# Kernel tuning notes

Hardware: AMD Instinct MI355X
Metric: run time of the kernel (lower is better)

Reference implementation:

```python
import jax, jax.numpy as jnp
import numpy as np

H = 8   # heads
C = 64  # per-head channels (gnn_hidden_dim)
HID = H * C  # 512
IN_CH = 6
EMB = 64
U, M = 16, 512
N_NODES = U * M  # 8192
N_EDGES = 131072


def _tconv(x, src, dst, Wq, bq, Wk, bk, Wv, bv, Ws, bs):
    """PyG TransformerConv (concat=True, root_weight=True, beta=False, eval mode)."""
    N = x.shape[0]
    q = (x @ Wq + bq).reshape(N, H, C)
    k = (x @ Wk + bk).reshape(N, H, C)
    v = (x @ Wv + bv).reshape(N, H, C)
    # per-edge attention scores: query at dst (target i), key at src (source j)
    score = jnp.einsum('ehc,ehc->eh', q[dst], k[src]) / jnp.sqrt(jnp.float32(C))
    # segment softmax over incoming edges of each dst node
    mx = jax.ops.segment_max(score, dst, num_segments=N)
    ex = jnp.exp(score - mx[dst])
    denom = jax.ops.segment_sum(ex, dst, num_segments=N)
    alpha = ex / (denom[dst] + 1e-16)  # [E, H]
    msg = alpha[..., None] * v[src]    # [E, H, C]
    out = jax.ops.segment_sum(msg, dst, num_segments=N).reshape(N, HID)
    return out + x @ Ws + bs  # root/skip connection


def setup_inputs() -> dict:
    key = jax.random.key(0)
    ks = iter(jax.random.split(key, 64))
    s = 0.05

    def lin(k, i, o):
        k1, k2 = jax.random.split(k)
        return (jax.random.normal(k1, (i, o), jnp.float32) * s,
                jax.random.normal(k2, (o,), jnp.float32) * s)

    inp = {}
    inp['mission_coords'] = jax.random.uniform(next(ks), (M, 2), jnp.float32)
    inp['uavs_info'] = jax.random.uniform(next(ks), (U, 2), jnp.float32)
    inp['speeds'] = jax.random.uniform(next(ks), (U,), jnp.float32)
    inp['dist_matrix'] = jax.random.uniform(next(ks), (U, M), jnp.float32)
    inp['timetogo_matrix'] = jax.random.uniform(next(ks), (U, M), jnp.float32)
    inp['action_mask'] = jax.random.randint(next(ks), (U, M), 0, 2, jnp.int32)
    inp['edge_index'] = jax.random.randint(next(ks), (2, N_EDGES), 0, N_NODES, jnp.int64)
    inp['batch'] = jnp.zeros((U,), jnp.int64)

    # layer 0 (in=6)
    inp['Wq0'], inp['bq0'] = lin(next(ks), IN_CH, HID)
    inp['Wk0'], inp['bk0'] = lin(next(ks), IN_CH, HID)
    inp['Wv0'], inp['bv0'] = lin(next(ks), IN_CH, HID)
    inp['Ws0'], inp['bs0'] = lin(next(ks), IN_CH, HID)
    # layers 1..3 stacked (in=512)
    for nm in ['Wq', 'Wk', 'Wv', 'Ws']:
        Ws_, bs_ = [], []
        for _ in range(3):
            w, b = lin(next(ks), HID, HID)
            Ws_.append(w); bs_.append(b)
        inp[nm] = jnp.stack(Ws_)
        inp['b' + nm[1:].lower()] = jnp.stack(bs_)
    inp['Wout'], inp['bout'] = lin(next(ks), HID, EMB)
    inp['Wa1'], inp['ba1'] = lin(next(ks), EMB + 3, 128)
    inp['Wa2'], inp['ba2'] = lin(next(ks), 128, 1)
    inp['Wc1'], inp['bc1'] = lin(next(ks), EMB + 3, 128)
    inp['Wc2'], inp['bc2'] = lin(next(ks), 128, 1)
    return inp


def reference(mission_coords, uavs_info, speeds, dist_matrix, timetogo_matrix,
              action_mask, edge_index, batch,
              Wq0, bq0, Wk0, bk0, Wv0, bv0, Ws0, bs0,
              Wq, bq, Wk, bk, Wv, bv, Ws, bs,
              Wout, bout, Wa1, ba1, Wa2, ba2, Wc1, bc1, Wc2, bc2):
    u, m = uavs_info.shape[0], mission_coords.shape[0]
    mc = jnp.broadcast_to(mission_coords[None], (u, m, 2))
    mask_e = action_mask[..., None].astype(jnp.float32)
    sp_e = jnp.broadcast_to(speeds[:, None, None], (u, m, 1))
    x = jnp.concatenate([mc, mask_e, sp_e, dist_matrix[..., None],
                         timetogo_matrix[..., None]], axis=-1).reshape(u * m, IN_CH)
    src, dst = edge_index[0], edge_index[1]
    x = jax.nn.relu(_tconv(x, src, dst, Wq0, bq0, Wk0, bk0, Wv0, bv0, Ws0, bs0))
    for l in range(3):
        x = jax.nn.relu(_tconv(x, src, dst, Wq[l], bq[l], Wk[l], bk[l],
                               Wv[l], bv[l], Ws[l], bs[l]))
    x = x @ Wout + bout  # [U*M, EMB]
    uav_emb = x.reshape(u, m, EMB).sum(axis=1)  # sum pooling over missions
    combined = jnp.concatenate([uavs_info, uav_emb, speeds[:, None]], axis=-1)
    logits = jax.nn.relu(combined @ Wa1 + ba1) @ Wa2 + ba2  # [U, 1]
    action_probs = jax.nn.softmax(logits, axis=-1)
    state_values = (jax.nn.relu(combined @ Wc1 + bc1) @ Wc2 + bc2).squeeze()
    return action_probs, state_values
```

## Files before the change

### kernel.cpp

```cpp
#include <hip/hip_runtime.h>
#include <hip/hip_bf16.h>
#include <math.h>

#define NNODES 8192
#define NEDGES 131072
#define HID    512
#define UU     16
#define MM     512
#define NQKVS  2048

#if __has_builtin(__builtin_amdgcn_cvt_pk_f32_fp8) && __has_builtin(__builtin_amdgcn_cvt_pk_fp8_f32)
#define HAVE_FP8 1
#else
#define HAVE_FP8 0
#endif

#define KSCALE 16.0f
#define KISCALE (0.125f / 16.0f)

typedef __attribute__((ext_vector_type(8))) short bf16x8;
typedef __attribute__((ext_vector_type(4))) float f32x4;
typedef __attribute__((ext_vector_type(2))) float f32x2;

__device__ __forceinline__ float bf2f(ushort u) {
    return __uint_as_float(((unsigned)u) << 16);
}
__device__ __forceinline__ ushort f2bf(float f) {
    unsigned x = __float_as_uint(f);
    return (ushort)((x + 0x7fffu + ((x >> 16) & 1u)) >> 16);
}

__global__ __launch_bounds__(256) void k_wt(
    const float* __restrict__ Wq, const float* __restrict__ Wk,
    const float* __restrict__ Wv, const float* __restrict__ Ws,
    ushort* __restrict__ Wt)
{
    __shared__ float tile[64][65];
    int z = blockIdx.z;
    int l = z >> 2, which = z & 3;
    const float* src = (which == 0 ? Wq : which == 1 ? Wk : which == 2 ? Wv : Ws)
                       + (size_t)l * HID * HID;
    int k0 = blockIdx.x * 64, c0 = blockIdx.y * 64;
    int t = threadIdx.x;
#pragma unroll
    for (int i = 0; i < 16; ++i) {
        int idx = i * 256 + t;
        int r = idx >> 6, c = idx & 63;
        tile[r][c] = src[(size_t)(k0 + r) * HID + c0 + c];
    }
    __syncthreads();
    ushort* dst = Wt + ((size_t)l * NQKVS + which * HID + c0) * HID + k0;
#pragma unroll
    for (int i = 0; i < 16; ++i) {
        int idx = i * 256 + t;
        int r = idx >> 6, c = idx & 63;
        dst[(size_t)r * HID + c] = f2bf(tile[c][r]);
    }
}

__global__ __launch_bounds__(256) void k_bias(
    const float* __restrict__ bq, const float* __restrict__ bk,
    const float* __restrict__ bv, const float* __restrict__ bs,
    float* __restrict__ bcat)
{
    int i = blockIdx.x * 256 + threadIdx.x;
    int l = i >> 11, j = i & 2047;
    int which = j >> 9, jj = j & 511;
    const float* b = which == 0 ? bq : which == 1 ? bk : which == 2 ? bv : bs;
    bcat[i] = b[l * HID + jj];
}

__global__ __launch_bounds__(256) void k_lin0(
    const float* __restrict__ mc, const float* __restrict__ speeds,
    const float* __restrict__ dist, const float* __restrict__ ttg,
    const int* __restrict__ mask,
    const float* __restrict__ Wq0, const float* __restrict__ bq0,
    const float* __restrict__ Wk0, const float* __restrict__ bk0,
    const float* __restrict__ Wv0, const float* __restrict__ bv0,
    const float* __restrict__ Ws0, const float* __restrict__ bs0,
    ushort* __restrict__ Y, unsigned char* __restrict__ Kf8)
{
    int n = blockIdx.x;
    int u = n >> 9, m = n & 511;
    float x[6];
    x[0] = mc[m * 2 + 0];
    x[1] = mc[m * 2 + 1];
    x[2] = (float)mask[u * MM + m];
    x[3] = speeds[u];
    x[4] = dist[u * MM + m];
    x[5] = ttg[u * MM + m];

    int j = threadIdx.x;
    int col0 = j * 8;
    int which = col0 >> 9, jj = col0 & 511;
    const float* W = which == 0 ? Wq0 : which == 1 ? Wk0 : which == 2 ? Wv0 : Ws0;
    const float* b = which == 0 ? bq0 : which == 1 ? bk0 : which == 2 ? bv0 : bs0;
    float s[8];
#pragma unroll
    for (int uu = 0; uu < 8; ++uu) s[uu] = b[jj + uu];
#pragma unroll
    for (int t = 0; t < 6; ++t)
#pragma unroll
        for (int uu = 0; uu < 8; ++uu)
            s[uu] = fmaf(x[t], W[t * HID + jj + uu], s[uu]);
    bf16x8 o8;
#pragma unroll
    for (int uu = 0; uu < 8; ++uu) o8[uu] = (short)f2bf(s[uu]);
    *(bf16x8*)(Y + (size_t)n * NQKVS + col0) = o8;
#if HAVE_FP8
    if (which == 1) {
        int w0 = __builtin_amdgcn_cvt_pk_fp8_f32(s[0] * KSCALE, s[1] * KSCALE, 0, false);
        w0     = __builtin_amdgcn_cvt_pk_fp8_f32(s[2] * KSCALE, s[3] * KSCALE, w0, true);
        int w1 = __builtin_amdgcn_cvt_pk_fp8_f32(s[4] * KSCALE, s[5] * KSCALE, 0, false);
        w1     = __builtin_amdgcn_cvt_pk_fp8_f32(s[6] * KSCALE, s[7] * KSCALE, w1, true);
        uint2 uu2; uu2.x = (unsigned)w0; uu2.y = (unsigned)w1;
        *(uint2*)(Kf8 + (size_t)n * HID + jj) = uu2;
    }
#endif
}

#define GBM 256
#define GBN 256
#define GBK 64
#define MATB 32768
#define BUFB (2 * MATB)

#define VMCNT(n) asm volatile("s_waitcnt vmcnt(" #n ")" ::: "memory")

__device__ __forceinline__ void stage_tile256(
    const ushort* __restrict__ Ag, const ushort* __restrict__ Bg,
    char* __restrict__ buf, int t)
{
#pragma unroll
    for (int h = 0; h < 8; ++h) {
        int slot = h * 512 + t;
        const ushort* src = (h < 4) ? Ag : Bg;
        int s = slot & 2047;
        int row = s >> 3, kqs = s & 7;
        int kq = kqs ^ (row & 7);
        __builtin_amdgcn_global_load_lds(
            (const __attribute__((address_space(1))) void*)(src + (size_t)row * HID + kq * 8),
            (__attribute__((address_space(3))) void*)(buf + slot * 16), 16, 0, 0);
    }
}

__global__ __launch_bounds__(512, 1) void k_gemm(
    const ushort* __restrict__ A,
    const ushort* __restrict__ Bt,
    const float* __restrict__ bias,
    ushort* __restrict__ Y,
    unsigned char* __restrict__ Kf8)
{
    extern __shared__ char lds[];
    const int t = threadIdx.x;
    const int bid = blockIdx.x;
    const int xcd = bid & 7;
    const int ii  = bid >> 3;
    const int mi  = (xcd << 2) | (ii & 3);
    const int ni  = ii >> 2;
    const int m0 = mi * GBM, n0 = ni * GBN;

    const int wid = t >> 6, lane = t & 63;
    const int wr = wid >> 2, wc = wid & 3;
    const int l15 = lane & 15, lkq = lane >> 4;

    f32x4 acc[8][4] = {};

    const ushort* Ab = A + (size_t)m0 * HID;
    const ushort* Bb = Bt + (size_t)n0 * HID;

    stage_tile256(Ab, Bb, lds, t);
    stage_tile256(Ab + GBK, Bb + GBK, lds + BUFB, t);

    const int NKT = HID / GBK;
#pragma unroll
    for (int T = 0; T < NKT; ++T) {
        if (T < NKT - 1) { VMCNT(8); } else { VMCNT(0); }
        __builtin_amdgcn_s_barrier();
        __builtin_amdgcn_sched_barrier(0);
        const char* la = lds + (T & 1) * BUFB;
        const char* lb = la + MATB;
#pragma unroll
        for (int kh = 0; kh < 2; ++kh) {
            const int kq = kh * 4 + lkq;
            const int sw = (kq ^ (l15 & 7)) << 4;
            bf16x8 a[8], b[4];
#pragma unroll
            for (int i = 0; i < 8; ++i)
                a[i] = *(const bf16x8*)(la + (wr * 128 + i * 16 + l15) * 128 + sw);
#pragma unroll
            for (int j = 0; j < 4; ++j)
                b[j] = *(const bf16x8*)(lb + (wc * 64 + j * 16 + l15) * 128 + sw);
            __builtin_amdgcn_s_setprio(1);
#pragma unroll
            for (int i = 0; i < 8; ++i)
#pragma unroll
                for (int j = 0; j < 4; ++j)
                    acc[i][j] = __builtin_amdgcn_mfma_f32_16x16x32_bf16(a[i], b[j], acc[i][j], 0, 0, 0);
            __builtin_amdgcn_s_setprio(0);
        }
        __builtin_amdgcn_s_barrier();
        __builtin_amdgcn_sched_barrier(0);
        if (T + 2 < NKT)
            stage_tile256(Ab + (T + 2) * GBK, Bb + (T + 2) * GBK,
                          lds + (T & 1) * BUFB, t);
    }

    const bool kquad = ((n0 >> 9) == 1);
#pragma unroll
    for (int i = 0; i < 8; ++i) {
        int row = m0 + wr * 128 + i * 16 + lkq * 4;
#pragma unroll
        for (int j = 0; j < 4; ++j) {
            int col = n0 + wc * 64 + j * 16 + l15;
            float bc = bias[col];
            f32x4 r = acc[i][j];
#pragma unroll
            for (int g = 0; g < 4; ++g) {
                float val = r[g] + bc;
                Y[(size_t)(row + g) * NQKVS + col] = f2bf(val);
#if HAVE_FP8
                if (kquad) {
                    int pk = __builtin_amdgcn_cvt_pk_fp8_f32(val * KSCALE, val * KSCALE, 0, false);
                    Kf8[(size_t)(row + g) * HID + (col - 512)] = (unsigned char)(pk & 0xff);
                }
#endif
            }
        }
    }
}

__global__ __launch_bounds__(256) void k_hist(const int* __restrict__ dst, int* __restrict__ cnt)
{
    int e = blockIdx.x * blockDim.x + threadIdx.x;
    if (e < NEDGES) atomicAdd(&cnt[dst[e]], 1);
}

__global__ __launch_bounds__(256) void k_scan(const int* __restrict__ cnt, int* __restrict__ indptr)
{
    __shared__ int sums[256];
    __shared__ int offs[256];
    int t = threadIdx.x;
    int base = t * 32;
    int s = 0;
    for (int i = 0; i < 32; ++i) s += cnt[base + i];
    sums[t] = s;
    __syncthreads();
    if (t == 0) {
        int run = 0;
        for (int i = 0; i < 256; ++i) { offs[i] = run; run += sums[i]; }
    }
    __syncthreads();
    int off = offs[t];
    for (int i = 0; i < 32; ++i) { indptr[base + i] = off; off += cnt[base + i]; }
    if (t == 255) indptr[NNODES] = off;
}

__global__ __launch_bounds__(256) void k_scatter(
    const int* __restrict__ src, const int* __restrict__ dst,
    const int* __restrict__ indptr, int* __restrict__ cursor, int* __restrict__ ssrc)
{
    int e = blockIdx.x * blockDim.x + threadIdx.x;
    if (e >= NEDGES) return;
    int d = dst[e];
    int p = atomicAdd(&cursor[d], 1);
    ssrc[indptr[d] + p] = src[e];
}

__global__ __launch_bounds__(256) void k_attn(
    const int* __restrict__ indptr, const int* __restrict__ ssrc,
    const ushort* __restrict__ Y,
    const unsigned char* __restrict__ Kf8,
    ushort* __restrict__ X)
{
    int n = blockIdx.x * 4 + (threadIdx.x >> 6);
    if (n >= NNODES) return;
    int l = threadIdx.x & 63;
    int cbase = l * 8;
    const ushort* yq = Y + (size_t)n * NQKVS + cbase;
    float qf[8];
    {
        bf16x8 q8 = *(const bf16x8*)yq;
#pragma unroll
        for (int j = 0; j < 8; ++j) qf[j] = bf2f((ushort)q8[j]);
    }
    float mrun = -INFINITY, ssum = 0.f;
    float acc[8] = {};
    int e0 = indptr[n], e1 = indptr[n + 1];
#if HAVE_FP8
    uint2 ka = {}, kb = {};
#else
    bf16x8 ka = {}, kb = {};
#endif
    bf16x8 va = {}, vb = {};
    if (e0 < e1) {
        int s = ssrc[e0];
#if HAVE_FP8
        ka = *(const uint2*)(Kf8 + (size_t)s * HID + cbase);
#else
        ka = *(const bf16x8*)(Y + (size_t)s * NQKVS + 512 + cbase);
#endif
        va = *(const bf16x8*)(Y + (size_t)s * NQKVS + 1024 + cbase);
    }
    if (e0 + 1 < e1) {
        int s = ssrc[e0 + 1];
#if HAVE_FP8
        kb = *(const uint2*)(Kf8 + (size_t)s * HID + cbase);
#else
        kb = *(const bf16x8*)(Y + (size_t)s * NQKVS + 512 + cbase);
#endif
        vb = *(const bf16x8*)(Y + (size_t)s * NQKVS + 1024 + cbase);
    }
    for (int e = e0; e < e1; ++e) {
        auto k8 = ka; bf16x8 v8 = va;
        ka = kb; va = vb;
        int en = e + 2;
        if (en < e1) {
            int s = ssrc[en];
#if HAVE_FP8
            kb = *(const uint2*)(Kf8 + (size_t)s * HID + cbase);
#else
            kb = *(const bf16x8*)(Y + (size_t)s * NQKVS + 512 + cbase);
#endif
            vb = *(const bf16x8*)(Y + (size_t)s * NQKVS + 1024 + cbase);
        }
        float part = 0.f;
#if HAVE_FP8
        {
            f32x2 k01 = __builtin_amdgcn_cvt_pk_f32_fp8((int)k8.x, false);
            f32x2 k23 = __builtin_amdgcn_cvt_pk_f32_fp8((int)k8.x, true);
            f32x2 k45 = __builtin_amdgcn_cvt_pk_f32_fp8((int)k8.y, false);
            f32x2 k67 = __builtin_amdgcn_cvt_pk_f32_fp8((int)k8.y, true);
            part = fmaf(qf[0], k01.x, part); part = fmaf(qf[1], k01.y, part);
            part = fmaf(qf[2], k23.x, part); part = fmaf(qf[3], k23.y, part);
            part = fmaf(qf[4], k45.x, part); part = fmaf(qf[5], k45.y, part);
            part = fmaf(qf[6], k67.x, part); part = fmaf(qf[7], k67.y, part);
        }
#else
#pragma unroll
        for (int j = 0; j < 8; ++j) part = fmaf(qf[j], bf2f((ushort)k8[j]), part);
#endif
        part += __shfl_xor(part, 1);
        part += __shfl_xor(part, 2);
        part += __shfl_xor(part, 4);
#if HAVE_FP8
        float score = part * KISCALE;
#else
        float score = part * 0.125f;
#endif
        float mnew = fmaxf(mrun, score);
        float sc = __expf(mrun - mnew);
        float p = __expf(score - mnew);
        ssum = ssum * sc + p;
#pragma unroll
        for (int j = 0; j < 8; ++j)
            acc[j] = fmaf(acc[j], sc, p * bf2f((ushort)v8[j]));
        mrun = mnew;
    }
    float inv = ssum > 0.f ? 1.f / ssum : 0.f;
    bf16x8 o8;
#pragma unroll
    for (int j = 0; j < 8; ++j) {
        float o = fmaxf(fmaf(acc[j], inv, bf2f(yq[1536 + j])), 0.f);
        o8[j] = (short)f2bf(o);
    }
    *(bf16x8*)(X + (size_t)n * HID + cbase) = o8;
}

__global__ __launch_bounds__(512) void k_pool(const ushort* __restrict__ X, float* __restrict__ xsumP)
{
    int u = blockIdx.x;
    int pp = blockIdx.y;
    int c = threadIdx.x;
    const ushort* base = X + ((size_t)u * MM + pp * 64) * HID + c;
    float s = 0.f;
    for (int m = 0; m < 64; ++m) s += bf2f(base[(size_t)m * HID]);
    xsumP[((size_t)u * 8 + pp) * HID + c] = s;
}

__global__ __launch_bounds__(512) void k_emb(
    const float* __restrict__ xsumP, const float* __restrict__ Wout,
    const float* __restrict__ bout, float* __restrict__ emb)
{
    __shared__ float xs[HID];
    int u = blockIdx.x, c = threadIdx.x;
    float s = 0.f;
#pragma unroll
    for (int p = 0; p < 8; ++p) s += xsumP[((size_t)u * 8 + p) * HID + c];
    xs[c] = s;
    __syncthreads();
    if (c < 64) {
        float a = 0.f;
        for (int i = 0; i < HID; ++i) a = fmaf(xs[i], Wout[i * 64 + c], a);
        emb[u * 64 + c] = a + 512.0f * bout[c];
    }
}

__global__ __launch_bounds__(128) void k_head(
    const float* __restrict__ uavs, const float* __restrict__ speeds,
    const float* __restrict__ emb,
    const float* __restrict__ Wc1, const float* __restrict__ bc1,
    const float* __restrict__ Wc2, const float* __restrict__ bc2,
    float* __restrict__ out)
{
    __shared__ float comb[67];
    __shared__ float red[128];
    int u = blockIdx.x, t = threadIdx.x;
    if (t < 2) comb[t] = uavs[u * 2 + t];
    else if (t < 66) comb[t] = emb[u * 64 + (t - 2)];
    else if (t == 66) comb[t] = speeds[u];
    __syncthreads();
    float a = bc1[t];
    for (int i = 0; i < 67; ++i) a = fmaf(comb[i], Wc1[i * 128 + t], a);
    a = fmaxf(a, 0.f);
    red[t] = a * Wc2[t];
    __syncthreads();
    for (int sft = 64; sft > 0; sft >>= 1) {
        if (t < sft) red[t] += red[t + sft];
        __syncthreads();
    }
    if (t == 0) {
        out[u]      = 1.0f;
        out[16 + u] = red[0] + bc2[0];
    }
}

extern "C" void kernel_launch(void* const* d_in, const int* in_sizes, int n_in,
                              void* d_out, int out_size, void* d_ws, size_t ws_size,
                              hipStream_t stream)
{
    const float* mission_coords = (const float*)d_in[0];
    const float* uavs_info      = (const float*)d_in[1];
    const float* speeds         = (const float*)d_in[2];
    const float* dist_matrix    = (const float*)d_in[3];
    const float* timetogo       = (const float*)d_in[4];
    const int*   action_mask    = (const int*)d_in[5];
    const int*   edge_index     = (const int*)d_in[6];
    const float* Wq0 = (const float*)d_in[8];  const float* bq0 = (const float*)d_in[9];
    const float* Wk0 = (const float*)d_in[10]; const float* bk0 = (const float*)d_in[11];
    const float* Wv0 = (const float*)d_in[12]; const float* bv0 = (const float*)d_in[13];
    const float* Ws0 = (const float*)d_in[14]; const float* bs0 = (const float*)d_in[15];
    const float* Wq  = (const float*)d_in[16]; const float* bq  = (const float*)d_in[17];
    const float* Wk  = (const float*)d_in[18]; const float* bk  = (const float*)d_in[19];
    const float* Wv  = (const float*)d_in[20]; const float* bv  = (const float*)d_in[21];
    const float* Ws  = (const float*)d_in[22]; const float* bs  = (const float*)d_in[23];
    const float* Wout = (const float*)d_in[24]; const float* bout = (const float*)d_in[25];
    const float* Wc1 = (const float*)d_in[30]; const float* bc1 = (const float*)d_in[31];
    const float* Wc2 = (const float*)d_in[32]; const float* bc2 = (const float*)d_in[33];
    float* out = (float*)d_out;

    const int* e_src = edge_index;
    const int* e_dst = edge_index + NEDGES;

    char* p = (char*)d_ws;
    ushort* Ybf = (ushort*)p;  p += (size_t)NNODES * NQKVS * 2;
    ushort* Xbf = (ushort*)p;  p += (size_t)NNODES * HID * 2;
    ushort* Wt  = (ushort*)p;  p += (size_t)3 * NQKVS * HID * 2;
    unsigned char* Kf8 = (unsigned char*)p; p += (size_t)NNODES * HID;
    float* bcat = (float*)p;   p += (size_t)3 * NQKVS * 4;
    float* xsumP = (float*)p;  p += (size_t)UU * 8 * HID * 4;
    float* emb  = (float*)p;   p += (size_t)UU * 64 * 4;
    int* cnt    = (int*)p;     p += (size_t)NNODES * 4;
    int* indptr = (int*)p;     p += (size_t)(NNODES + 1) * 4;
    int* cursor = (int*)p;     p += (size_t)NNODES * 4;
    int* ssrc   = (int*)p;     p += (size_t)NEDGES * 4;

    hipMemsetAsync(cnt, 0, NNODES * sizeof(int), stream);
    hipMemsetAsync(cursor, 0, NNODES * sizeof(int), stream);

    static bool attr_done = false;
    if (!attr_done) {
        hipFuncSetAttribute((const void*)k_gemm,
                            hipFuncAttributeMaxDynamicSharedMemorySize, 131072);
        attr_done = true;
    }

    k_wt<<<dim3(8, 8, 12), 256, 0, stream>>>(Wq, Wk, Wv, Ws, Wt);
    k_bias<<<3 * NQKVS / 256, 256, 0, stream>>>(bq, bk, bv, bs, bcat);
    k_hist<<<NEDGES / 256, 256, 0, stream>>>(e_dst, cnt);
    k_scan<<<1, 256, 0, stream>>>(cnt, indptr);
    k_scatter<<<NEDGES / 256, 256, 0, stream>>>(e_src, e_dst, indptr, cursor, ssrc);

    k_lin0<<<NNODES, 256, 0, stream>>>(mission_coords, speeds, dist_matrix, timetogo,
                                       action_mask, Wq0, bq0, Wk0, bk0, Wv0, bv0,
                                       Ws0, bs0, Ybf, Kf8);
    k_attn<<<NNODES / 4, 256, 0, stream>>>(indptr, ssrc, Ybf, Kf8, Xbf);

    const int ngblocks = (NNODES / GBM) * (NQKVS / GBN);
    for (int l = 0; l < 3; ++l) {
        k_gemm<<<ngblocks, 512, 131072, stream>>>(Xbf, Wt + (size_t)l * NQKVS * HID,
                                                  bcat + l * NQKVS, Ybf, Kf8);
        k_attn<<<NNODES / 4, 256, 0, stream>>>(indptr, ssrc, Ybf, Kf8, Xbf);
    }

    k_pool<<<dim3(UU, 8), 512, 0, stream>>>(Xbf, xsumP);
    k_emb<<<UU, 512, 0, stream>>>(xsumP, Wout, bout, emb);
    k_head<<<UU, 128, 0, stream>>>(uavs_info, speeds, emb, Wc1, bc1, Wc2, bc2, out);
}
```

Before: 281.2 us.

## Shrink GEMM tiles, deepen attention prefetch, fuse small setup and head kernels

The GEMM moves from 256x256x64 tiles with 512 threads and 128KB dynamic LDS to 128x128x32 tiles with 256 threads, static LDS and four blocks per CU, using a new LDS swizzle that interleaves A and B rows. The aim is more blocks in flight and better latency hiding. The cost is less operand reuse per block and more global traffic. The attention loop now prefetches four edges ahead instead of two. Several small launches are also merged: weight transpose with bias concat, embedding with head, and the two memsets into one. The scan is rewritten with wave shuffles.

```diff
diff --git a/kernel.cpp b/kernel.cpp
--- a/kernel.cpp
+++ b/kernel.cpp
@@ -30,18 +30,31 @@
     return (ushort)((x + 0x7fffu + ((x >> 16) & 1u)) >> 16);
 }
 
-__global__ __launch_bounds__(256) void k_wt(
+__global__ __launch_bounds__(256) void k_wtb(
     const float* __restrict__ Wq, const float* __restrict__ Wk,
     const float* __restrict__ Wv, const float* __restrict__ Ws,
-    ushort* __restrict__ Wt)
+    const float* __restrict__ bq, const float* __restrict__ bk,
+    const float* __restrict__ bv, const float* __restrict__ bs,
+    ushort* __restrict__ Wt, float* __restrict__ bcat)
 {
     __shared__ float tile[64][65];
     int z = blockIdx.z;
+    int t = threadIdx.x;
+    if (z == 12) {
+        int id = blockIdx.y * 8 + blockIdx.x;
+        if (id < 24) {
+            int i = id * 256 + t;
+            int l = i >> 11, j = i & 2047;
+            int which = j >> 9, jj = j & 511;
+            const float* b = which == 0 ? bq : which == 1 ? bk : which == 2 ? bv : bs;
+            bcat[i] = b[l * HID + jj];
+        }
+        return;
+    }
     int l = z >> 2, which = z & 3;
     const float* src = (which == 0 ? Wq : which == 1 ? Wk : which == 2 ? Wv : Ws)
                        + (size_t)l * HID * HID;
     int k0 = blockIdx.x * 64, c0 = blockIdx.y * 64;
-    int t = threadIdx.x;
 #pragma unroll
     for (int i = 0; i < 16; ++i) {
         int idx = i * 256 + t;
@@ -56,18 +69,6 @@
         int r = idx >> 6, c = idx & 63;
         dst[(size_t)r * HID + c] = f2bf(tile[c][r]);
     }
-}
-
-__global__ __launch_bounds__(256) void k_bias(
-    const float* __restrict__ bq, const float* __restrict__ bk,
-    const float* __restrict__ bv, const float* __restrict__ bs,
-    float* __restrict__ bcat)
-{
-    int i = blockIdx.x * 256 + threadIdx.x;
-    int l = i >> 11, j = i & 2047;
-    int which = j >> 9, jj = j & 511;
-    const float* b = which == 0 ? bq : which == 1 ? bk : which == 2 ? bv : bs;
-    bcat[i] = b[l * HID + jj];
 }
 
 __global__ __launch_bounds__(256) void k_lin0(
@@ -119,97 +120,99 @@
 #endif
 }
 
-#define GBM 256
-#define GBN 256
-#define GBK 64
-#define MATB 32768
-#define BUFB (2 * MATB)
+#define GBM 128
+#define GBN 128
+#define GBK 32
+#define BUF32 16384
 
 #define VMCNT(n) asm volatile("s_waitcnt vmcnt(" #n ")" ::: "memory")
 
-__device__ __forceinline__ void stage_tile256(
+__device__ __forceinline__ void stage32(
     const ushort* __restrict__ Ag, const ushort* __restrict__ Bg,
     char* __restrict__ buf, int t)
 {
 #pragma unroll
-    for (int h = 0; h < 8; ++h) {
-        int slot = h * 512 + t;
-        const ushort* src = (h < 4) ? Ag : Bg;
-        int s = slot & 2047;
-        int row = s >> 3, kqs = s & 7;
-        int kq = kqs ^ (row & 7);
+    for (int i = 0; i < 4; ++i) {
+        int slot = i * 256 + t;
+        int row  = slot >> 3;
+        int sl8  = slot & 7;
+        int h    = sl8 >> 2;
+        int kqs  = sl8 & 3;
+        int hA   = (row >> 2) & 1;
+        int kq   = kqs ^ (row & 3);
+        const ushort* src = (h == hA ? Ag : Bg) + (size_t)row * HID + kq * 8;
         __builtin_amdgcn_global_load_lds(
-            (const __attribute__((address_space(1))) void*)(src + (size_t)row * HID + kq * 8),
+            (const __attribute__((address_space(1))) void*)src,
             (__attribute__((address_space(3))) void*)(buf + slot * 16), 16, 0, 0);
     }
 }
 
-__global__ __launch_bounds__(512, 1) void k_gemm(
+__global__ __launch_bounds__(256, 4) void k_gemm(
     const ushort* __restrict__ A,
     const ushort* __restrict__ Bt,
     const float* __restrict__ bias,
     ushort* __restrict__ Y,
     unsigned char* __restrict__ Kf8)
 {
-    extern __shared__ char lds[];
+    __shared__ char lds[2 * BUF32];
     const int t = threadIdx.x;
     const int bid = blockIdx.x;
     const int xcd = bid & 7;
     const int ii  = bid >> 3;
-    const int mi  = (xcd << 2) | (ii & 3);
-    const int ni  = ii >> 2;
+    const int mi  = (xcd << 3) | (ii & 7);
+    const int ni  = ii >> 3;
     const int m0 = mi * GBM, n0 = ni * GBN;
 
     const int wid = t >> 6, lane = t & 63;
-    const int wr = wid >> 2, wc = wid & 3;
+    const int wr = wid >> 1, wc = wid & 1;
     const int l15 = lane & 15, lkq = lane >> 4;
 
-    f32x4 acc[8][4] = {};
+    f32x4 acc[4][4] = {};
 
     const ushort* Ab = A + (size_t)m0 * HID;
     const ushort* Bb = Bt + (size_t)n0 * HID;
 
-    stage_tile256(Ab, Bb, lds, t);
-    stage_tile256(Ab + GBK, Bb + GBK, lds + BUFB, t);
+    stage32(Ab, Bb, lds, t);
+    stage32(Ab + GBK, Bb + GBK, lds + BUF32, t);
 
     const int NKT = HID / GBK;
 #pragma unroll
     for (int T = 0; T < NKT; ++T) {
-        if (T < NKT - 1) { VMCNT(8); } else { VMCNT(0); }
+        if (T < NKT - 1) { VMCNT(4); } else { VMCNT(0); }
         __builtin_amdgcn_s_barrier();
         __builtin_amdgcn_sched_barrier(0);
-        const char* la = lds + (T & 1) * BUFB;
-        const char* lb = la + MATB;
-#pragma unroll
-        for (int kh = 0; kh < 2; ++kh) {
-            const int kq = kh * 4 + lkq;
-            const int sw = (kq ^ (l15 & 7)) << 4;
-            bf16x8 a[8], b[4];
-#pragma unroll
-            for (int i = 0; i < 8; ++i)
-                a[i] = *(const bf16x8*)(la + (wr * 128 + i * 16 + l15) * 128 + sw);
+        const char* lb_ = lds + (T & 1) * BUF32;
+        bf16x8 a[4], b[4];
+#pragma unroll
+        for (int i = 0; i < 4; ++i) {
+            int row = wr * 64 + i * 16 + l15;
+            a[i] = *(const bf16x8*)(lb_ + row * 128 + ((row & 4) << 4)
+                                    + ((lkq ^ (row & 3)) << 4));
+        }
+#pragma unroll
+        for (int j = 0; j < 4; ++j) {
+            int row = wc * 64 + j * 16 + l15;
+            b[j] = *(const bf16x8*)(lb_ + row * 128 + (((row & 4) ^ 4) << 4)
+                                    + ((lkq ^ (row & 3)) << 4));
+        }
+        __builtin_amdgcn_s_setprio(1);
+#pragma unroll
+        for (int i = 0; i < 4; ++i)
 #pragma unroll
             for (int j = 0; j < 4; ++j)
-                b[j] = *(const bf16x8*)(lb + (wc * 64 + j * 16 + l15) * 128 + sw);
-            __builtin_amdgcn_s_setprio(1);
-#pragma unroll
-            for (int i = 0; i < 8; ++i)
-#pragma unroll
-                for (int j = 0; j < 4; ++j)
-                    acc[i][j] = __builtin_amdgcn_mfma_f32_16x16x32_bf16(a[i], b[j], acc[i][j], 0, 0, 0);
-            __builtin_amdgcn_s_setprio(0);
-        }
+                acc[i][j] = __builtin_amdgcn_mfma_f32_16x16x32_bf16(a[i], b[j], acc[i][j], 0, 0, 0);
+        __builtin_amdgcn_s_setprio(0);
         __builtin_amdgcn_s_barrier();
         __builtin_amdgcn_sched_barrier(0);
         if (T + 2 < NKT)
-            stage_tile256(Ab + (T + 2) * GBK, Bb + (T + 2) * GBK,
-                          lds + (T & 1) * BUFB, t);
+            stage32(Ab + (T + 2) * GBK, Bb + (T + 2) * GBK,
+                    lds + (T & 1) * BUF32, t);
     }
 
     const bool kquad = ((n0 >> 9) == 1);
 #pragma unroll
-    for (int i = 0; i < 8; ++i) {
-        int row = m0 + wr * 128 + i * 16 + lkq * 4;
+    for (int i = 0; i < 4; ++i) {
+        int row = m0 + wr * 64 + i * 16 + lkq * 4;
 #pragma unroll
         for (int j = 0; j < 4; ++j) {
             int col = n0 + wc * 64 + j * 16 + l15;
@@ -236,24 +239,35 @@
     if (e < NEDGES) atomicAdd(&cnt[dst[e]], 1);
 }
 
-__global__ __launch_bounds__(256) void k_scan(const int* __restrict__ cnt, int* __restrict__ indptr)
-{
-    __shared__ int sums[256];
-    __shared__ int offs[256];
+__global__ __launch_bounds__(1024) void k_scan(const int* __restrict__ cnt, int* __restrict__ indptr)
+{
+    __shared__ int wsum[16];
+    __shared__ int woff[16];
     int t = threadIdx.x;
-    int base = t * 32;
+    int base = t * 8;
+    int v[8];
     int s = 0;
-    for (int i = 0; i < 32; ++i) s += cnt[base + i];
-    sums[t] = s;
+#pragma unroll
+    for (int i = 0; i < 8; ++i) { v[i] = cnt[base + i]; s += v[i]; }
+    int lane = t & 63, w = t >> 6;
+    int incl = s;
+#pragma unroll
+    for (int off = 1; off < 64; off <<= 1) {
+        int u = __shfl_up(incl, off);
+        if (lane >= off) incl += u;
+    }
+    if (lane == 63) wsum[w] = incl;
     __syncthreads();
     if (t == 0) {
         int run = 0;
-        for (int i = 0; i < 256; ++i) { offs[i] = run; run += sums[i]; }
-    }
-    __syncthreads();
-    int off = offs[t];
-    for (int i = 0; i < 32; ++i) { indptr[base + i] = off; off += cnt[base + i]; }
-    if (t == 255) indptr[NNODES] = off;
+#pragma unroll
+        for (int i = 0; i < 16; ++i) { woff[i] = run; run += wsum[i]; }
+    }
+    __syncthreads();
+    int run = woff[w] + incl - s;
+#pragma unroll
+    for (int i = 0; i < 8; ++i) { indptr[base + i] = run; run += v[i]; }
+    if (t == 1023) indptr[NNODES] = run;
 }
 
 __global__ __launch_bounds__(256) void k_scatter(
@@ -287,75 +301,61 @@
     float mrun = -INFINITY, ssum = 0.f;
     float acc[8] = {};
     int e0 = indptr[n], e1 = indptr[n + 1];
+
 #if HAVE_FP8
-    uint2 ka = {}, kb = {};
+    uint2 kA = {}, kB = {}, kC = {}, kD = {};
+#define KLOAD(K_, s_) K_ = *(const uint2*)(Kf8 + (size_t)(s_) * HID + cbase)
 #else
-    bf16x8 ka = {}, kb = {};
+    bf16x8 kA = {}, kB = {}, kC = {}, kD = {};
+#define KLOAD(K_, s_) K_ = *(const bf16x8*)(Y + (size_t)(s_) * NQKVS + 512 + cbase)
 #endif
-    bf16x8 va = {}, vb = {};
-    if (e0 < e1) {
-        int s = ssrc[e0];
+    bf16x8 vA = {}, vB = {}, vC = {}, vD = {};
+
+#define LOADKV(K_, V_, idx) \
+    if ((idx) < e1) { int s_ = ssrc[idx]; KLOAD(K_, s_); \
+        V_ = *(const bf16x8*)(Y + (size_t)s_ * NQKVS + 1024 + cbase); }
+
 #if HAVE_FP8
-        ka = *(const uint2*)(Kf8 + (size_t)s * HID + cbase);
+#define DOTK(K_, part) { \
+        f32x2 k01 = __builtin_amdgcn_cvt_pk_f32_fp8((int)K_.x, false); \
+        f32x2 k23 = __builtin_amdgcn_cvt_pk_f32_fp8((int)K_.x, true); \
+        f32x2 k45 = __builtin_amdgcn_cvt_pk_f32_fp8((int)K_.y, false); \
+        f32x2 k67 = __builtin_amdgcn_cvt_pk_f32_fp8((int)K_.y, true); \
+        part = fmaf(qf[0], k01.x, part); part = fmaf(qf[1], k01.y, part); \
+        part = fmaf(qf[2], k23.x, part); part = fmaf(qf[3], k23.y, part); \
+        part = fmaf(qf[4], k45.x, part); part = fmaf(qf[5], k45.y, part); \
+        part = fmaf(qf[6], k67.x, part); part = fmaf(qf[7], k67.y, part); }
+#define SCOREMUL KISCALE
 #else
-        ka = *(const bf16x8*)(Y + (size_t)s * NQKVS + 512 + cbase);
+#define DOTK(K_, part) { _Pragma("unroll") \
+        for (int j = 0; j < 8; ++j) part = fmaf(qf[j], bf2f((ushort)K_[j]), part); }
+#define SCOREMUL 0.125f
 #endif
-        va = *(const bf16x8*)(Y + (size_t)s * NQKVS + 1024 + cbase);
-    }
-    if (e0 + 1 < e1) {
-        int s = ssrc[e0 + 1];
-#if HAVE_FP8
-        kb = *(const uint2*)(Kf8 + (size_t)s * HID + cbase);
-#else
-        kb = *(const bf16x8*)(Y + (size_t)s * NQKVS + 512 + cbase);
-#endif
-        vb = *(const bf16x8*)(Y + (size_t)s * NQKVS + 1024 + cbase);
-    }
-    for (int e = e0; e < e1; ++e) {
-        auto k8 = ka; bf16x8 v8 = va;
-        ka = kb; va = vb;
-        int en = e + 2;
-        if (en < e1) {
-            int s = ssrc[en];
-#if HAVE_FP8
-            kb = *(const uint2*)(Kf8 + (size_t)s * HID + cbase);
-#else
-            kb = *(const bf16x8*)(Y + (size_t)s * NQKVS + 512 + cbase);
-#endif
-            vb = *(const bf16x8*)(Y + (size_t)s * NQKVS + 1024 + cbase);
-        }
-        float part = 0.f;
-#if HAVE_FP8
-        {
-            f32x2 k01 = __builtin_amdgcn_cvt_pk_f32_fp8((int)k8.x, false);
-            f32x2 k23 = __builtin_amdgcn_cvt_pk_f32_fp8((int)k8.x, true);
-            f32x2 k45 = __builtin_amdgcn_cvt_pk_f32_fp8((int)k8.y, false);
-            f32x2 k67 = __builtin_amdgcn_cvt_pk_f32_fp8((int)k8.y, true);
-            part = fmaf(qf[0], k01.x, part); part = fmaf(qf[1], k01.y, part);
-            part = fmaf(qf[2], k23.x, part); part = fmaf(qf[3], k23.y, part);
-            part = fmaf(qf[4], k45.x, part); part = fmaf(qf[5], k45.y, part);
-            part = fmaf(qf[6], k67.x, part); part = fmaf(qf[7], k67.y, part);
-        }
-#else
-#pragma unroll
-        for (int j = 0; j < 8; ++j) part = fmaf(qf[j], bf2f((ushort)k8[j]), part);
-#endif
-        part += __shfl_xor(part, 1);
-        part += __shfl_xor(part, 2);
-        part += __shfl_xor(part, 4);
-#if HAVE_FP8
-        float score = part * KISCALE;
-#else
-        float score = part * 0.125f;
-#endif
-        float mnew = fmaxf(mrun, score);
-        float sc = __expf(mrun - mnew);
-        float p = __expf(score - mnew);
-        ssum = ssum * sc + p;
-#pragma unroll
-        for (int j = 0; j < 8; ++j)
-            acc[j] = fmaf(acc[j], sc, p * bf2f((ushort)v8[j]));
-        mrun = mnew;
+
+#define PROC(K_, V_) { \
+        float part = 0.f; \
+        DOTK(K_, part); \
+        part += __shfl_xor(part, 1); \
+        part += __shfl_xor(part, 2); \
+        part += __shfl_xor(part, 4); \
+        float score = part * SCOREMUL; \
+        float mnew = fmaxf(mrun, score); \
+        float sc = __expf(mrun - mnew); \
+        float p = __expf(score - mnew); \
+        ssum = ssum * sc + p; \
+        _Pragma("unroll") \
+        for (int j = 0; j < 8; ++j) acc[j] = fmaf(acc[j], sc, p * bf2f((ushort)V_[j])); \
+        mrun = mnew; }
+
+    LOADKV(kA, vA, e0 + 0);
+    LOADKV(kB, vB, e0 + 1);
+    LOADKV(kC, vC, e0 + 2);
+    LOADKV(kD, vD, e0 + 3);
+    for (int e = e0; e < e1; e += 4) {
+        PROC(kA, vA); LOADKV(kA, vA, e + 4);
+        if (e + 1 < e1) { PROC(kB, vB); LOADKV(kB, vB, e + 5); }
+        if (e + 2 < e1) { PROC(kC, vC); LOADKV(kC, vC, e + 6); }
+        if (e + 3 < e1) { PROC(kD, vD); LOADKV(kD, vD, e + 7); }
     }
     float inv = ssum > 0.f ? 1.f / ssum : 0.f;
     bf16x8 o8;
@@ -378,11 +378,17 @@
     xsumP[((size_t)u * 8 + pp) * HID + c] = s;
 }
 
-__global__ __launch_bounds__(512) void k_emb(
+__global__ __launch_bounds__(512) void k_embhead(
     const float* __restrict__ xsumP, const float* __restrict__ Wout,
-    const float* __restrict__ bout, float* __restrict__ emb)
+    const float* __restrict__ bout,
+    const float* __restrict__ uavs, const float* __restrict__ speeds,
+    const float* __restrict__ Wc1, const float* __restrict__ bc1,
+    const float* __restrict__ Wc2, const float* __restrict__ bc2,
+    float* __restrict__ out)
 {
     __shared__ float xs[HID];
+    __shared__ float comb[67];
+    __shared__ float red[128];
     int u = blockIdx.x, c = threadIdx.x;
     float s = 0.f;
 #pragma unroll
@@ -392,34 +398,23 @@
     if (c < 64) {
         float a = 0.f;
         for (int i = 0; i < HID; ++i) a = fmaf(xs[i], Wout[i * 64 + c], a);
-        emb[u * 64 + c] = a + 512.0f * bout[c];
-    }
-}
-
-__global__ __launch_bounds__(128) void k_head(
-    const float* __restrict__ uavs, const float* __restrict__ speeds,
-    const float* __restrict__ emb,
-    const float* __restrict__ Wc1, const float* __restrict__ bc1,
-    const float* __restrict__ Wc2, const float* __restrict__ bc2,
-    float* __restrict__ out)
-{
-    __shared__ float comb[67];
-    __shared__ float red[128];
-    int u = blockIdx.x, t = threadIdx.x;
-    if (t < 2) comb[t] = uavs[u * 2 + t];
-    else if (t < 66) comb[t] = emb[u * 64 + (t - 2)];
-    else if (t == 66) comb[t] = speeds[u];
-    __syncthreads();
-    float a = bc1[t];
-    for (int i = 0; i < 67; ++i) a = fmaf(comb[i], Wc1[i * 128 + t], a);
-    a = fmaxf(a, 0.f);
-    red[t] = a * Wc2[t];
+        comb[2 + c] = a + 512.0f * bout[c];
+    }
+    if (c == 64) { comb[0] = uavs[u * 2]; comb[1] = uavs[u * 2 + 1]; }
+    if (c == 65) comb[66] = speeds[u];
+    __syncthreads();
+    if (c < 128) {
+        float a = bc1[c];
+        for (int i = 0; i < 67; ++i) a = fmaf(comb[i], Wc1[i * 128 + c], a);
+        a = fmaxf(a, 0.f);
+        red[c] = a * Wc2[c];
+    }
     __syncthreads();
     for (int sft = 64; sft > 0; sft >>= 1) {
-        if (t < sft) red[t] += red[t + sft];
+        if (c < sft) red[c] += red[c + sft];
         __syncthreads();
     }
-    if (t == 0) {
+    if (c == 0) {
         out[u]      = 1.0f;
         out[16 + u] = red[0] + bc2[0];
     }
@@ -459,26 +454,16 @@
     unsigned char* Kf8 = (unsigned char*)p; p += (size_t)NNODES * HID;
     float* bcat = (float*)p;   p += (size_t)3 * NQKVS * 4;
     float* xsumP = (float*)p;  p += (size_t)UU * 8 * HID * 4;
-    float* emb  = (float*)p;   p += (size_t)UU * 64 * 4;
     int* cnt    = (int*)p;     p += (size_t)NNODES * 4;
+    int* cursor = (int*)p;     p += (size_t)NNODES * 4;
     int* indptr = (int*)p;     p += (size_t)(NNODES + 1) * 4;
-    int* cursor = (int*)p;     p += (size_t)NNODES * 4;
     int* ssrc   = (int*)p;     p += (size_t)NEDGES * 4;
 
-    hipMemsetAsync(cnt, 0, NNODES * sizeof(int), stream);
-    hipMemsetAsync(cursor, 0, NNODES * sizeof(int), stream);
-
-    static bool attr_done = false;
-    if (!attr_done) {
-        hipFuncSetAttribute((const void*)k_gemm,
-                            hipFuncAttributeMaxDynamicSharedMemorySize, 131072);
-        attr_done = true;
-    }
-
-    k_wt<<<dim3(8, 8, 12), 256, 0, stream>>>(Wq, Wk, Wv, Ws, Wt);
-    k_bias<<<3 * NQKVS / 256, 256, 0, stream>>>(bq, bk, bv, bs, bcat);
+    hipMemsetAsync(cnt, 0, 2 * NNODES * sizeof(int), stream);
+
+    k_wtb<<<dim3(8, 8, 13), 256, 0, stream>>>(Wq, Wk, Wv, Ws, bq, bk, bv, bs, Wt, bcat);
     k_hist<<<NEDGES / 256, 256, 0, stream>>>(e_dst, cnt);
-    k_scan<<<1, 256, 0, stream>>>(cnt, indptr);
+    k_scan<<<1, 1024, 0, stream>>>(cnt, indptr);
     k_scatter<<<NEDGES / 256, 256, 0, stream>>>(e_src, e_dst, indptr, cursor, ssrc);
 
     k_lin0<<<NNODES, 256, 0, stream>>>(mission_coords, speeds, dist_matrix, timetogo,
@@ -488,12 +473,12 @@
 
     const int ngblocks = (NNODES / GBM) * (NQKVS / GBN);
     for (int l = 0; l < 3; ++l) {
-        k_gemm<<<ngblocks, 512, 131072, stream>>>(Xbf, Wt + (size_t)l * NQKVS * HID,
-                                                  bcat + l * NQKVS, Ybf, Kf8);
+        k_gemm<<<ngblocks, 256, 0, stream>>>(Xbf, Wt + (size_t)l * NQKVS * HID,
+                                             bcat + l * NQKVS, Ybf, Kf8);
         k_attn<<<NNODES / 4, 256, 0, stream>>>(indptr, ssrc, Ybf, Kf8, Xbf);
     }
 
     k_pool<<<dim3(UU, 8), 512, 0, stream>>>(Xbf, xsumP);
-    k_emb<<<UU, 512, 0, stream>>>(xsumP, Wout, bout, emb);
-    k_head<<<UU, 128, 0, stream>>>(uavs_info, speeds, emb, Wc1, bc1, Wc2, bc2, out);
-}
+    k_embhead<<<UU, 512, 0, stream>>>(xsumP, Wout, bout, uavs_info, speeds,
+                                      Wc1, bc1, Wc2, bc2, out);
+}
```

Result: slower. 293.2 us (+4.2%).
